# Kernel optimization log

Hardware: AMD Instinct MI355X
Metric: run time of the kernel (lower is better)

## Reference

```python
import jax, jax.numpy as jnp
import numpy as np

N_ENT = 50000
N_REL = 16
N_EDGE = 1000000
D = 64


def setup_inputs() -> dict:
    key = jax.random.key(0)
    ks = jax.random.split(key, 20)
    inp = {
        'ent_embed': jax.random.normal(ks[0], (N_ENT, D), jnp.float32) * 0.1,
        'rel_embed': jax.random.normal(ks[1], (N_REL, D), jnp.float32) * 0.1,
        'W_R': jax.random.normal(ks[2], (N_REL, D, D), jnp.float32) * 0.1,
        'W1_0': jax.random.normal(ks[3], (64, 64), jnp.float32) * 0.1,
        'b1_0': jax.random.normal(ks[4], (64,), jnp.float32) * 0.1,
        'W2_0': jax.random.normal(ks[5], (64, 64), jnp.float32) * 0.1,
        'b2_0': jax.random.normal(ks[6], (64,), jnp.float32) * 0.1,
        'W1_1': jax.random.normal(ks[7], (64, 32), jnp.float32) * 0.1,
        'b1_1': jax.random.normal(ks[8], (32,), jnp.float32) * 0.1,
        'W2_1': jax.random.normal(ks[9], (64, 32), jnp.float32) * 0.1,
        'b2_1': jax.random.normal(ks[10], (32,), jnp.float32) * 0.1,
        'W1_2': jax.random.normal(ks[11], (32, 16), jnp.float32) * 0.1,
        'b1_2': jax.random.normal(ks[12], (16,), jnp.float32) * 0.1,
        'W2_2': jax.random.normal(ks[13], (32, 16), jnp.float32) * 0.1,
        'b2_2': jax.random.normal(ks[14], (16,), jnp.float32) * 0.1,
        'src': jax.random.randint(ks[15], (N_EDGE,), 0, N_ENT, jnp.int32),
        'dst': jax.random.randint(ks[16], (N_EDGE,), 0, N_ENT, jnp.int32),
        'etype': jax.random.randint(ks[17], (N_EDGE,), 0, N_REL, jnp.int32),
    }
    return inp


def _l2_normalize(x, eps=1e-12):
    # matches torch F.normalize(p=2, dim=1)
    n = jnp.sqrt(jnp.sum(x * x, axis=1, keepdims=True))
    return x / jnp.maximum(n, eps)


def _kgat_forward(ent_embed, rel_embed, W_R, layer_params, src, dst, etype):
    N = ent_embed.shape[0]
    # --- compute_attention: per-relation TransR projection of all entities ---
    # equivalent to per-edge ent[src] @ W_R[type] without materializing [E, D, D]
    proj = jnp.einsum('nd,rde->rne', ent_embed, W_R)          # [R, N, D]
    r_mul_t = proj[etype, src]                                # [E, D] (tail = src)
    r_mul_h = proj[etype, dst]                                # [E, D] (head = dst)
    att = jnp.sum(r_mul_t * jnp.tanh(r_mul_h + rel_embed[etype]), axis=-1)  # [E]
    # edge softmax grouped by destination node
    m = jax.ops.segment_max(att, dst, num_segments=N)         # [N]
    e = jnp.exp(att - m[dst])
    s = jax.ops.segment_sum(e, dst, num_segments=N)           # [N]
    a = e / s[dst]                                            # [E]

    # --- cf_embedding: bi-interaction aggregator layers ---
    h = ent_embed
    all_embed = [h]
    for (W1, b1, W2, b2) in layer_params:
        msg = a[:, None] * h[src]                             # [E, d_in]
        N_h = jax.ops.segment_sum(msg, dst, num_segments=N)   # [N, d_in]
        out = (jax.nn.leaky_relu((h + N_h) @ W1 + b1, 0.01)
               + jax.nn.leaky_relu((h * N_h) @ W2 + b2, 0.01))
        h = out
        all_embed.append(_l2_normalize(out))
    return jnp.concatenate(all_embed, axis=1)                 # [N, 64+64+32+16=176]


def reference(ent_embed, rel_embed, W_R,
              W1_0, b1_0, W2_0, b2_0,
              W1_1, b1_1, W2_1, b2_1,
              W1_2, b1_2, W2_2, b2_2,
              src, dst, etype):
    layer_params = [(W1_0, b1_0, W2_0, b2_0),
                    (W1_1, b1_1, W2_1, b2_1),
                    (W1_2, b1_2, W2_2, b2_2)]
    return _kgat_forward(ent_embed, rel_embed, W_R, layer_params, src, dst, etype)
```

## Files before the change

kernel.cpp:

```cpp
#include <hip/hip_runtime.h>
#include <hip/hip_bf16.h>
#include <cmath>

#define N_ENT  50000
#define N_RELS 16
#define N_EDGE 1000000
#define DIM    64
#define OUT_STRIDE 176

typedef float f32x4 __attribute__((ext_vector_type(4)));
typedef short s16x8 __attribute__((ext_vector_type(8)));

__device__ inline void bf16x8_unpack(uint4 u, float* f) {
    f[0] = __uint_as_float((u.x & 0xffffu) << 16);
    f[1] = __uint_as_float(u.x & 0xffff0000u);
    f[2] = __uint_as_float((u.y & 0xffffu) << 16);
    f[3] = __uint_as_float(u.y & 0xffff0000u);
    f[4] = __uint_as_float((u.z & 0xffffu) << 16);
    f[5] = __uint_as_float(u.z & 0xffff0000u);
    f[6] = __uint_as_float((u.w & 0xffffu) << 16);
    f[7] = __uint_as_float(u.w & 0xffff0000u);
}

__device__ inline ushort f2bf(float x) {
    __hip_bfloat16 b = __float2bfloat16(x);
    return *(ushort*)&b;
}

__device__ inline uint cvt_pk_bf16(float lo, float hi) {
    uint r;
    asm("v_cvt_pk_bf16_f32 %0, %1, %2" : "=v"(r) : "v"(lo), "v"(hi));
    return r;
}

__device__ __host__ inline int pcol(int p) {
    int qp = (p >> 3) & 7;
    int k  = p & 7;
    return 16 * (k >> 1) + 2 * qp + (k & 1);
}

__global__ __launch_bounds__(256) void prep_hist_kernel(
        const float* __restrict__ ent,
        ushort* __restrict__ ent_pi,
        float* __restrict__ out,
        const int* __restrict__ dst, int* __restrict__ counts,
        int* __restrict__ off) {
    int i = blockIdx.x * blockDim.x + threadIdx.x;
    if (i < N_ENT * DIM) {
        float v = ent[i];
        ushort b = f2bf(v);
        int n = i >> 6, c = i & 63;
        int pos = ((c & 15) >> 1) * 8 + ((c >> 4) << 1) + (c & 1);
        ent_pi[(size_t)n * 64 + pos] = b;
        out[(size_t)n * OUT_STRIDE + c] = v;
    }
    if (i < N_EDGE) off[i] = atomicAdd(&counts[dst[i]], 1);
}

__global__ __launch_bounds__(256) void scan1_kernel(
        const int* __restrict__ counts, int* __restrict__ excl,
        int* __restrict__ bsum, int n) {
    __shared__ int sh[256];
    int t = threadIdx.x;
    int i = blockIdx.x * 256 + t;
    int c = (i < n) ? counts[i] : 0;
    sh[t] = c;
    __syncthreads();
    for (int off = 1; off < 256; off <<= 1) {
        int v = (t >= off) ? sh[t - off] : 0;
        __syncthreads();
        sh[t] += v;
        __syncthreads();
    }
    if (i < n) excl[i] = sh[t] - c;
    if (t == 255) bsum[blockIdx.x] = sh[255];
}

__global__ __launch_bounds__(256) void scan2_kernel(
        const int* __restrict__ bsum, int* __restrict__ boff,
        int* __restrict__ row_ptr, int nb, int n) {
    __shared__ int sh[256];
    int t = threadIdx.x;
    int v = (t < nb) ? bsum[t] : 0;
    sh[t] = v;
    __syncthreads();
    for (int off = 1; off < 256; off <<= 1) {
        int x = (t >= off) ? sh[t - off] : 0;
        __syncthreads();
        sh[t] += x;
        __syncthreads();
    }
    if (t < nb) boff[t] = sh[t] - v;
    if (t == nb - 1) row_ptr[n] = sh[t];
}

__global__ __launch_bounds__(256) void scan3_pos_kernel(
        const int* __restrict__ excl, const int* __restrict__ boff,
        int* __restrict__ row_ptr,
        const int* __restrict__ src, const int* __restrict__ dst,
        const int* __restrict__ etype, const int* __restrict__ off,
        unsigned long long* __restrict__ einfo) {
    int i = blockIdx.x * blockDim.x + threadIdx.x;
    if (i < N_ENT) row_ptr[i] = excl[i] + boff[i >> 8];
    if (i < N_EDGE) {
        int d = dst[i];
        int pos = excl[d] + boff[d >> 8] + off[i];
        unsigned long long info =
              (unsigned long long)(unsigned)src[i]
            | ((unsigned long long)(unsigned)d << 16)
            | ((unsigned long long)(unsigned)etype[i] << 32)
            | ((unsigned long long)(unsigned)pos << 36);
        einfo[i] = info;
    }
}

__global__ __launch_bounds__(256) void gz_mfma_kernel(
        const ushort* __restrict__ ent_pi,
        const float*  __restrict__ W_R,
        const float*  __restrict__ rel,
        ushort* __restrict__ Z) {
    __shared__ __align__(16) float lds[4][16 * 68 + 16];
    int lane = threadIdx.x & 63;
    int wv   = threadIdx.x >> 6;
    int m    = lane & 15;
    int q    = lane >> 4;
    int r    = blockIdx.y;
    int wid  = blockIdx.x * 4 + wv;
    int nw   = gridDim.x * 4;

    const float* Wr = W_R + (size_t)r * DIM * DIM;
    s16x8 b1[4][2], b2[4][2];
#pragma unroll
    for (int c = 0; c < 4; ++c)
#pragma unroll
        for (int ch = 0; ch < 2; ++ch)
#pragma unroll
            for (int j = 0; j < 8; ++j) {
                b1[c][ch][j] = (short)f2bf(Wr[pcol(ch * 32 + q * 8 + j) * DIM + c * 16 + m]);
                b2[c][ch][j] = (short)f2bf(Wr[(c * 16 + m) * DIM + ch * 32 + q * 8 + j]);
            }
    float relv[4];
#pragma unroll
    for (int c = 0; c < 4; ++c) relv[c] = rel[r * DIM + c * 16 + m];

    float* myLds = lds[wv];
    const int ntiles = N_ENT / 16;

    for (int t = wid; t < ntiles; t += nw) {
        int row0 = t * 16;
        const s16x8* arow = (const s16x8*)(ent_pi + (size_t)(row0 + m) * DIM);
        s16x8 a0 = arow[q];
        s16x8 a1 = arow[4 + q];
        f32x4 acc[4];
#pragma unroll
        for (int c = 0; c < 4; ++c) acc[c] = (f32x4){0.f, 0.f, 0.f, 0.f};
#pragma unroll
        for (int c = 0; c < 4; ++c) {
            acc[c] = __builtin_amdgcn_mfma_f32_16x16x32_bf16(a0, b1[c][0], acc[c], 0, 0, 0);
            acc[c] = __builtin_amdgcn_mfma_f32_16x16x32_bf16(a1, b1[c][1], acc[c], 0, 0, 0);
        }
#pragma unroll
        for (int c = 0; c < 4; ++c)
#pragma unroll
            for (int i = 0; i < 4; ++i) {
                float x = acc[c][i] + relv[c];
                float g = 1.f - 2.f / (__expf(2.f * x) + 1.f);
                myLds[(q * 4 + i) * 68 + c * 16 + m] = g;
            }
        union { uint u[4]; s16x8 v; } a2u[2];
#pragma unroll
        for (int ch = 0; ch < 2; ++ch) {
            const f32x4* gp = (const f32x4*)(myLds + m * 68 + ch * 32 + q * 8);
            f32x4 g0 = gp[0];
            f32x4 g1 = gp[1];
            a2u[ch].u[0] = cvt_pk_bf16(g0[0], g0[1]);
            a2u[ch].u[1] = cvt_pk_bf16(g0[2], g0[3]);
            a2u[ch].u[2] = cvt_pk_bf16(g1[0], g1[1]);
            a2u[ch].u[3] = cvt_pk_bf16(g1[2], g1[3]);
        }

        f32x4 zacc[4];
#pragma unroll
        for (int c = 0; c < 4; ++c) zacc[c] = (f32x4){0.f, 0.f, 0.f, 0.f};
#pragma unroll
        for (int c = 0; c < 4; ++c) {
            zacc[c] = __builtin_amdgcn_mfma_f32_16x16x32_bf16(a2u[0].v, b2[c][0], zacc[c], 0, 0, 0);
            zacc[c] = __builtin_amdgcn_mfma_f32_16x16x32_bf16(a2u[1].v, b2[c][1], zacc[c], 0, 0, 0);
        }

        float oth[4][4];
#pragma unroll
        for (int c = 0; c < 4; ++c)
#pragma unroll
            for (int i = 0; i < 4; ++i)
                oth[c][i] = __shfl_xor(zacc[c][i], 1, 64);
        int par = m & 1;
        uint wrd[4][4];
#pragma unroll
        for (int c = 0; c < 4; ++c)
#pragma unroll
            for (int i = 0; i < 4; ++i) {
                float lo = par ? oth[c][i] : zacc[c][i];
                float hi = par ? zacc[c][i] : oth[c][i];
                wrd[c][i] = cvt_pk_bf16(lo, hi);
            }
        uint4 W0, W1;
        ((uint*)&W0)[0] = par ? wrd[0][2] : wrd[0][0];
        ((uint*)&W0)[1] = par ? wrd[1][2] : wrd[1][0];
        ((uint*)&W0)[2] = par ? wrd[2][2] : wrd[2][0];
        ((uint*)&W0)[3] = par ? wrd[3][2] : wrd[3][0];
        ((uint*)&W1)[0] = par ? wrd[0][3] : wrd[0][1];
        ((uint*)&W1)[1] = par ? wrd[1][3] : wrd[1][1];
        ((uint*)&W1)[2] = par ? wrd[2][3] : wrd[2][1];
        ((uint*)&W1)[3] = par ? wrd[3][3] : wrd[3][1];
        int rowA = row0 + 4 * q + (par ? 2 : 0);
        ushort* zb = Z + ((size_t)r * N_ENT + rowA) * 64 + (m >> 1) * 8;
        *(uint4*)zb = W0;
        *(uint4*)(zb + 64) = W1;
    }
}

__global__ __launch_bounds__(256) void att_dot_kernel(
        const ushort* __restrict__ ent_pi,
        const ushort* __restrict__ Z,
        const unsigned long long* __restrict__ einfo,
        uint2* __restrict__ es_csr,
        int n_edge) {
    int tid  = blockIdx.x * blockDim.x + threadIdx.x;
    int lane = threadIdx.x & 63;
    int sub  = lane >> 3;
    int q    = lane & 7;
    int base = (tid >> 6) * 16;
    int e0 = base + sub;
    int e1 = base + 8 + sub;
    if (e0 >= n_edge) return;
    bool v1 = (e1 < n_edge);
    unsigned long long i0 = einfo[e0];
    unsigned long long i1 = v1 ? einfo[e1] : i0;

    int s0 = (int)(i0 & 0xffffu);
    int d0 = (int)((i0 >> 16) & 0xffffu);
    int r0 = (int)((i0 >> 32) & 0xfu);
    int p0 = (int)(i0 >> 36);
    int s1 = (int)(i1 & 0xffffu);
    int d1 = (int)((i1 >> 16) & 0xffffu);
    int r1 = (int)((i1 >> 32) & 0xfu);
    int p1 = (int)(i1 >> 36);

    uint4 uz0 = *(const uint4*)(Z + ((size_t)r0 * N_ENT + d0) * DIM + q * 8);
    uint4 ue0 = *(const uint4*)(ent_pi + (size_t)s0 * DIM + q * 8);
    uint4 uz1 = *(const uint4*)(Z + ((size_t)r1 * N_ENT + d1) * DIM + q * 8);
    uint4 ue1 = *(const uint4*)(ent_pi + (size_t)s1 * DIM + q * 8);

    float z0[8], w0[8], z1[8], w1[8];
    bf16x8_unpack(uz0, z0);
    bf16x8_unpack(ue0, w0);
    bf16x8_unpack(uz1, z1);
    bf16x8_unpack(ue1, w1);

    float pr0 = 0.f, pr1 = 0.f;
#pragma unroll
    for (int j = 0; j < 8; ++j) {
        pr0 = fmaf(w0[j], z0[j], pr0);
        pr1 = fmaf(w1[j], z1[j], pr1);
    }
    pr0 += __shfl_xor(pr0, 1, 64);
    pr1 += __shfl_xor(pr1, 1, 64);
    pr0 += __shfl_xor(pr0, 2, 64);
    pr1 += __shfl_xor(pr1, 2, 64);
    pr0 += __shfl_xor(pr0, 4, 64);
    pr1 += __shfl_xor(pr1, 4, 64);

    if (q == 0) {
        es_csr[p0] = make_uint2(__float_as_uint(pr0), (unsigned)s0);
        if (v1) es_csr[p1] = make_uint2(__float_as_uint(pr1), (unsigned)s1);
    }
}

__global__ __launch_bounds__(256) void stats_kernel(
        const int* __restrict__ row_ptr, const uint2* __restrict__ es_csr,
        float2* __restrict__ stats, int n_node) {
    int wid  = (blockIdx.x * blockDim.x + threadIdx.x) >> 6;
    int lane = threadIdx.x & 63;
    if (wid >= n_node) return;
    int start = row_ptr[wid], end = row_ptr[wid + 1];

    float m = -INFINITY;
    for (int i = start + lane; i < end; i += 64)
        m = fmaxf(m, __uint_as_float(es_csr[i].x));
#pragma unroll
    for (int off = 32; off > 0; off >>= 1)
        m = fmaxf(m, __shfl_xor(m, off, 64));

    float ssum = 0.f;
    for (int i = start + lane; i < end; i += 64)
        ssum += __expf(__uint_as_float(es_csr[i].x) - m);
#pragma unroll
    for (int off = 32; off > 0; off >>= 1)
        ssum += __shfl_xor(ssum, off, 64);

    if (lane == 0)
        stats[wid] = make_float2(m, (end > start) ? (1.0f / ssum) : 0.f);
}

__global__ __launch_bounds__(256) void agg64_kernel(
        const ushort* __restrict__ tab,
        const uint2* __restrict__ es_csr,
        const int* __restrict__ row_ptr,
        const float2* __restrict__ stats,
        float* __restrict__ N_h, int n_node) {
    int wid  = (blockIdx.x * blockDim.x + threadIdx.x) >> 6;
    int lane = threadIdx.x & 63;
    if (wid >= n_node) return;
    int q   = lane & 7;
    int sub = lane >> 3;

    int start = row_ptr[wid], end = row_ptr[wid + 1];
    float2 st = stats[wid];
    float mx = st.x, inv = st.y;
    float acc[8];
#pragma unroll
    for (int j = 0; j < 8; ++j) acc[j] = 0.f;

    for (int p = start + sub; p < end; p += 8) {
        uint2 es = es_csr[p];
        float av = __expf(__uint_as_float(es.x) - mx);
        int   si = (int)es.y;
        uint4 u  = *(const uint4*)(tab + (size_t)si * 64 + q * 8);
        float g[8];
        bf16x8_unpack(u, g);
#pragma unroll
        for (int j = 0; j < 8; ++j) acc[j] = fmaf(av, g[j], acc[j]);
    }
#pragma unroll
    for (int mask = 8; mask < 64; mask <<= 1)
#pragma unroll
        for (int j = 0; j < 8; ++j)
            acc[j] += __shfl_xor(acc[j], mask, 64);

    if (sub == 0) {
        float* dstp = N_h + (size_t)wid * 64 + q * 8;
        *(float4*)(dstp)     = (float4){acc[0] * inv, acc[1] * inv, acc[2] * inv, acc[3] * inv};
        *(float4*)(dstp + 4) = (float4){acc[4] * inv, acc[5] * inv, acc[6] * inv, acc[7] * inv};
    }
}

__global__ __launch_bounds__(256) void agg32_kernel(
        const ushort* __restrict__ tab,
        const uint2* __restrict__ es_csr,
        const int* __restrict__ row_ptr,
        const float2* __restrict__ stats,
        float* __restrict__ N_h, int n_node) {
    int wid  = (blockIdx.x * blockDim.x + threadIdx.x) >> 6;
    int lane = threadIdx.x & 63;
    if (wid >= n_node) return;
    int q   = lane & 3;
    int sub = lane >> 2;

    int start = row_ptr[wid], end = row_ptr[wid + 1];
    float2 st = stats[wid];
    float mx = st.x, inv = st.y;
    float acc[8];
#pragma unroll
    for (int j = 0; j < 8; ++j) acc[j] = 0.f;

    for (int p = start + sub; p < end; p += 16) {
        uint2 es = es_csr[p];
        float av = __expf(__uint_as_float(es.x) - mx);
        int   si = (int)es.y;
        uint4 u  = *(const uint4*)(tab + (size_t)si * 32 + q * 8);
        float g[8];
        bf16x8_unpack(u, g);
#pragma unroll
        for (int j = 0; j < 8; ++j) acc[j] = fmaf(av, g[j], acc[j]);
    }
#pragma unroll
    for (int mask = 4; mask < 64; mask <<= 1)
#pragma unroll
        for (int j = 0; j < 8; ++j)
            acc[j] += __shfl_xor(acc[j], mask, 64);

    if (sub == 0) {
        float* dstp = N_h + (size_t)wid * 32 + q * 8;
        *(float4*)(dstp)     = (float4){acc[0] * inv, acc[1] * inv, acc[2] * inv, acc[3] * inv};
        *(float4*)(dstp + 4) = (float4){acc[4] * inv, acc[5] * inv, acc[6] * inv, acc[7] * inv};
    }
}

template <int D_IN, int D_OUT, bool PERM>
__global__ __launch_bounds__(256) void mlp_mfma_kernel(
        const ushort* __restrict__ h,
        const float* __restrict__ N_h,
        const float* __restrict__ W1, const float* __restrict__ b1,
        const float* __restrict__ W2, const float* __restrict__ b2,
        ushort* __restrict__ ho,
        float* __restrict__ out_buf, int out_col) {
    constexpr int CH = D_IN / 32;
    constexpr int CT = D_OUT / 16;

    int lane = threadIdx.x & 63;
    int m    = lane & 15;
    int q    = lane >> 4;
    int wid  = blockIdx.x * (blockDim.x >> 6) + (threadIdx.x >> 6);
    int nw   = gridDim.x * (blockDim.x >> 6);

    s16x8 bu[CT][CH], bv[CT][CH];
#pragma unroll
    for (int c = 0; c < CT; ++c)
#pragma unroll
        for (int ch = 0; ch < CH; ++ch)
#pragma unroll
            for (int j = 0; j < 8; ++j) {
                int p = ch * 32 + q * 8 + j;
                int k = PERM ? pcol(p) : p;
                bu[c][ch][j] = (short)f2bf(W1[k * D_OUT + c * 16 + m]);
                bv[c][ch][j] = (short)f2bf(W2[k * D_OUT + c * 16 + m]);
            }

    const int ntiles = N_ENT / 16;
    for (int t = wid; t < ntiles; t += nw) {
        int row0 = t * 16;
        s16x8 au[CH], av[CH];
#pragma unroll
        for (int ch = 0; ch < CH; ++ch) {
            uint4 hu = *(const uint4*)(h + (size_t)(row0 + m) * D_IN + ch * 32 + q * 8);
            float hv8[8];
            bf16x8_unpack(hu, hv8);
            const float4* np = (const float4*)(N_h + (size_t)(row0 + m) * D_IN + ch * 32 + q * 8);
            float4 na = np[0], nb = np[1];
            float nv[8] = {na.x, na.y, na.z, na.w, nb.x, nb.y, nb.z, nb.w};
#pragma unroll
            for (int j = 0; j < 8; ++j) {
                au[ch][j] = (short)f2bf(hv8[j] + nv[j]);
                av[ch][j] = (short)f2bf(hv8[j] * nv[j]);
            }
        }

        f32x4 accu[CT], accv[CT];
#pragma unroll
        for (int c = 0; c < CT; ++c) {
            accu[c] = (f32x4){0.f, 0.f, 0.f, 0.f};
            accv[c] = (f32x4){0.f, 0.f, 0.f, 0.f};
        }
#pragma unroll
        for (int c = 0; c < CT; ++c)
#pragma unroll
            for (int ch = 0; ch < CH; ++ch) {
                accu[c] = __builtin_amdgcn_mfma_f32_16x16x32_bf16(au[ch], bu[c][ch], accu[c], 0, 0, 0);
                accv[c] = __builtin_amdgcn_mfma_f32_16x16x32_bf16(av[ch], bv[c][ch], accv[c], 0, 0, 0);
            }

        float res[CT][4];
        float sq[4] = {0.f, 0.f, 0.f, 0.f};
#pragma unroll
        for (int c = 0; c < CT; ++c) {
            float bb1 = b1[c * 16 + m];
            float bb2 = b2[c * 16 + m];
#pragma unroll
            for (int i = 0; i < 4; ++i) {
                float o1 = accu[c][i] + bb1;
                float o2 = accv[c][i] + bb2;
                float r1 = (o1 >= 0.f) ? o1 : 0.01f * o1;
                float r2 = (o2 >= 0.f) ? o2 : 0.01f * o2;
                float rr = r1 + r2;
                res[c][i] = rr;
                sq[i] = fmaf(rr, rr, sq[i]);
            }
        }
#pragma unroll
        for (int mask = 1; mask < 16; mask <<= 1)
#pragma unroll
            for (int i = 0; i < 4; ++i)
                sq[i] += __shfl_xor(sq[i], mask, 64);

#pragma unroll
        for (int i = 0; i < 4; ++i) {
            int row = row0 + q * 4 + i;
            float inv = 1.f / fmaxf(sqrtf(sq[i]), 1e-12f);
#pragma unroll
            for (int c = 0; c < CT; ++c) {
                int col = c * 16 + m;
                out_buf[(size_t)row * OUT_STRIDE + out_col + col] = res[c][i] * inv;
                if (ho) ho[(size_t)row * D_OUT + col] = f2bf(res[c][i]);
            }
        }
    }
}

extern "C" void kernel_launch(void* const* d_in, const int* in_sizes, int n_in,
                              void* d_out, int out_size, void* d_ws, size_t ws_size,
                              hipStream_t stream) {
    const float* ent  = (const float*)d_in[0];
    const float* rel  = (const float*)d_in[1];
    const float* W_R  = (const float*)d_in[2];
    const float* W1_0 = (const float*)d_in[3];
    const float* b1_0 = (const float*)d_in[4];
    const float* W2_0 = (const float*)d_in[5];
    const float* b2_0 = (const float*)d_in[6];
    const float* W1_1 = (const float*)d_in[7];
    const float* b1_1 = (const float*)d_in[8];
    const float* W2_1 = (const float*)d_in[9];
    const float* b2_1 = (const float*)d_in[10];
    const float* W1_2 = (const float*)d_in[11];
    const float* b1_2 = (const float*)d_in[12];
    const float* W2_2 = (const float*)d_in[13];
    const float* b2_2 = (const float*)d_in[14];
    const int*   src   = (const int*)d_in[15];
    const int*   dst   = (const int*)d_in[16];
    const int*   etype = (const int*)d_in[17];
    float* out = (float*)d_out;

    char* w = (char*)d_ws;
    uint2*  es_csr  = (uint2*)w;  w += (size_t)N_EDGE * 8;
    int*    counts  = (int*)w;    w += (size_t)(N_ENT + 64) * 4;
    int*    row_ptr = (int*)w;    w += (size_t)(N_ENT + 64) * 4;
    float2* stats   = (float2*)w; w += (size_t)(N_ENT + 64) * 8;
    int*    excl    = (int*)w;    w += (size_t)(N_ENT + 64) * 4;
    int*    bsum    = (int*)w;    w += 256 * 4;
    int*    boff    = (int*)w;    w += 256 * 4;
    ushort* ent_pi  = (ushort*)w; w += (size_t)N_ENT * 64 * 2;
    ushort* h1      = (ushort*)w; w += (size_t)N_ENT * 64 * 2;
    ushort* h2      = (ushort*)w; w += (size_t)N_ENT * 32 * 2;
    float*  N_h     = (float*)w;  w += (size_t)N_ENT * 64 * 4;
    ushort* Z       = (ushort*)w;
    (void)ws_size;

    int* off = (int*)Z;
    unsigned long long* einfo = (unsigned long long*)N_h;

    hipMemsetAsync(counts, 0, (size_t)N_ENT * 4, stream);

    const int nb = (N_ENT + 255) / 256;

    prep_hist_kernel<<<(N_ENT * DIM + 255) / 256, 256, 0, stream>>>(
        ent, ent_pi, out, dst, counts, off);
    scan1_kernel<<<nb, 256, 0, stream>>>(counts, excl, bsum, N_ENT);
    scan2_kernel<<<1, 256, 0, stream>>>(bsum, boff, row_ptr, nb, N_ENT);
    scan3_pos_kernel<<<(N_EDGE + 255) / 256, 256, 0, stream>>>(
        excl, boff, row_ptr, src, dst, etype, off, einfo);

    gz_mfma_kernel<<<dim3(96, N_RELS), 256, 0, stream>>>(ent_pi, W_R, rel, Z);
    att_dot_kernel<<<(N_EDGE / 16 * 64 + 255) / 256, 256, 0, stream>>>(
        ent_pi, Z, einfo, es_csr, N_EDGE);

    stats_kernel<<<(N_ENT + 3) / 4, 256, 0, stream>>>(row_ptr, es_csr, stats, N_ENT);

    const int aggGrid = (N_ENT + 3) / 4;
    const int mlpGrid = 782;

    agg64_kernel<<<aggGrid, 256, 0, stream>>>(ent_pi, es_csr, row_ptr, stats, N_h, N_ENT);
    mlp_mfma_kernel<64, 64, true><<<mlpGrid, 256, 0, stream>>>(
        ent_pi, N_h, W1_0, b1_0, W2_0, b2_0, h1, out, 64);

    agg64_kernel<<<aggGrid, 256, 0, stream>>>(h1, es_csr, row_ptr, stats, N_h, N_ENT);
    mlp_mfma_kernel<64, 32, false><<<mlpGrid, 256, 0, stream>>>(
        h1, N_h, W1_1, b1_1, W2_1, b2_1, h2, out, 128);

    agg32_kernel<<<aggGrid, 256, 0, stream>>>(h2, es_csr, row_ptr, stats, N_h, N_ENT);
    mlp_mfma_kernel<32, 16, false><<<mlpGrid, 256, 0, stream>>>(
        h2, N_h, W1_2, b1_2, W2_2, b2_2, nullptr, out, 160);
}
```

Baseline: 416.9 us.

## Scatter edge info into CSR order and process four edges per wave group

The edge-info records are now scattered into destination-sorted CSR position during the scan step instead of storing the position in the record. The attention dot kernel therefore reads einfo and writes es_csr sequentially, and consecutive edges share a destination so Z reads gain locality. Each 8-lane group also handles four edges instead of two, which adds memory-level parallelism. The cost is a scattered 8-byte write in scan3, and bounds checks for partial tails were removed, which is safe only because N_EDGE is a multiple of 32.

```diff
diff --git a/kernel.cpp b/kernel.cpp
--- a/kernel.cpp
+++ b/kernel.cpp
@@ -108,9 +108,8 @@
         unsigned long long info =
               (unsigned long long)(unsigned)src[i]
             | ((unsigned long long)(unsigned)d << 16)
-            | ((unsigned long long)(unsigned)etype[i] << 32)
-            | ((unsigned long long)(unsigned)pos << 36);
-        einfo[i] = info;
+            | ((unsigned long long)(unsigned)etype[i] << 32);
+        einfo[pos] = info;
     }
 }
 
@@ -230,50 +229,54 @@
     int lane = threadIdx.x & 63;
     int sub  = lane >> 3;
     int q    = lane & 7;
-    int base = (tid >> 6) * 16;
-    int e0 = base + sub;
-    int e1 = base + 8 + sub;
-    if (e0 >= n_edge) return;
-    bool v1 = (e1 < n_edge);
-    unsigned long long i0 = einfo[e0];
-    unsigned long long i1 = v1 ? einfo[e1] : i0;
-
-    int s0 = (int)(i0 & 0xffffu);
-    int d0 = (int)((i0 >> 16) & 0xffffu);
-    int r0 = (int)((i0 >> 32) & 0xfu);
-    int p0 = (int)(i0 >> 36);
-    int s1 = (int)(i1 & 0xffffu);
-    int d1 = (int)((i1 >> 16) & 0xffffu);
-    int r1 = (int)((i1 >> 32) & 0xfu);
-    int p1 = (int)(i1 >> 36);
-
-    uint4 uz0 = *(const uint4*)(Z + ((size_t)r0 * N_ENT + d0) * DIM + q * 8);
-    uint4 ue0 = *(const uint4*)(ent_pi + (size_t)s0 * DIM + q * 8);
-    uint4 uz1 = *(const uint4*)(Z + ((size_t)r1 * N_ENT + d1) * DIM + q * 8);
-    uint4 ue1 = *(const uint4*)(ent_pi + (size_t)s1 * DIM + q * 8);
-
-    float z0[8], w0[8], z1[8], w1[8];
-    bf16x8_unpack(uz0, z0);
-    bf16x8_unpack(ue0, w0);
-    bf16x8_unpack(uz1, z1);
-    bf16x8_unpack(ue1, w1);
-
-    float pr0 = 0.f, pr1 = 0.f;
-#pragma unroll
-    for (int j = 0; j < 8; ++j) {
-        pr0 = fmaf(w0[j], z0[j], pr0);
-        pr1 = fmaf(w1[j], z1[j], pr1);
-    }
-    pr0 += __shfl_xor(pr0, 1, 64);
-    pr1 += __shfl_xor(pr1, 1, 64);
-    pr0 += __shfl_xor(pr0, 2, 64);
-    pr1 += __shfl_xor(pr1, 2, 64);
-    pr0 += __shfl_xor(pr0, 4, 64);
-    pr1 += __shfl_xor(pr1, 4, 64);
+    int base = (tid >> 6) * 32;
+    if (base >= n_edge) return;
+
+    int e[4];
+    unsigned long long inf[4];
+#pragma unroll
+    for (int k = 0; k < 4; ++k) {
+        e[k] = base + k * 8 + sub;
+        inf[k] = einfo[e[k]];
+    }
+
+    int s[4], p_r[4], p_d[4];
+#pragma unroll
+    for (int k = 0; k < 4; ++k) {
+        s[k]   = (int)(inf[k] & 0xffffu);
+        p_d[k] = (int)((inf[k] >> 16) & 0xffffu);
+        p_r[k] = (int)((inf[k] >> 32) & 0xfu);
+    }
+
+    uint4 uz[4], ue[4];
+#pragma unroll
+    for (int k = 0; k < 4; ++k) {
+        uz[k] = *(const uint4*)(Z + ((size_t)p_r[k] * N_ENT + p_d[k]) * DIM + q * 8);
+        ue[k] = *(const uint4*)(ent_pi + (size_t)s[k] * DIM + q * 8);
+    }
+
+    float pr[4];
+#pragma unroll
+    for (int k = 0; k < 4; ++k) {
+        float zv[8], ev[8];
+        bf16x8_unpack(uz[k], zv);
+        bf16x8_unpack(ue[k], ev);
+        float p = 0.f;
+#pragma unroll
+        for (int j = 0; j < 8; ++j) p = fmaf(ev[j], zv[j], p);
+        pr[k] = p;
+    }
+#pragma unroll
+    for (int k = 0; k < 4; ++k) {
+        pr[k] += __shfl_xor(pr[k], 1, 64);
+        pr[k] += __shfl_xor(pr[k], 2, 64);
+        pr[k] += __shfl_xor(pr[k], 4, 64);
+    }
 
     if (q == 0) {
-        es_csr[p0] = make_uint2(__float_as_uint(pr0), (unsigned)s0);
-        if (v1) es_csr[p1] = make_uint2(__float_as_uint(pr1), (unsigned)s1);
+#pragma unroll
+        for (int k = 0; k < 4; ++k)
+            es_csr[e[k]] = make_uint2(__float_as_uint(pr[k]), (unsigned)s[k]);
     }
 }
 
@@ -540,7 +543,7 @@
         excl, boff, row_ptr, src, dst, etype, off, einfo);
 
     gz_mfma_kernel<<<dim3(96, N_RELS), 256, 0, stream>>>(ent_pi, W_R, rel, Z);
-    att_dot_kernel<<<(N_EDGE / 16 * 64 + 255) / 256, 256, 0, stream>>>(
+    att_dot_kernel<<<((N_EDGE + 31) / 32 * 64 + 255) / 256, 256, 0, stream>>>(
         ent_pi, Z, einfo, es_csr, N_EDGE);
 
     stats_kernel<<<(N_ENT + 3) / 4, 256, 0, stream>>>(row_ptr, es_csr, stats, N_ENT);
```

After: 387.4 us. 1.08x faster.
